# Optimization experiments

Hardware: AMD Instinct MI355X
Metric: run time of the kernel (lower is better)

## Reference

```python
import jax, jax.numpy as jnp
import numpy as np
from math import factorial

# ----- hyperparams (mirror init_kwargs) -----
HIDDEN = [(32,0,1),(32,0,-1),(8,1,1),(8,1,-1),(4,2,1),(4,2,-1)]  # (mul, l, parity)
SCALAR = [(32,0,1)]
SH_IRR = [(1,0,1),(1,1,-1),(1,2,1)]  # spherical harmonics 0e+1o+2e
EMB, NUM_RBF, R_MAX, MLP_DIM, D_IN = 32, 16, 10.0, 256, 64
N_NODES, N_EDGES, N_GRAPHS = 2048, 8192, 8
EDGE_FEATS_DIM = NUM_RBF + 2*EMB

def _slices(irs):
    s, o = [], 0
    for m, l, _ in irs:
        s.append(o); o += m*(2*l+1)
    return s

def _su2_cg(j1, j2, j3, m1, m2, m3):
    if m1 + m2 != m3:
        return 0.0
    f = factorial
    pref = ((2*j3+1)*f(j3+j1-j2)*f(j3-j1+j2)*f(j1+j2-j3)/f(j1+j2+j3+1))**0.5
    pref *= (f(j3+m3)*f(j3-m3)*f(j1-m1)*f(j1+m1)*f(j2-m2)*f(j2+m2))**0.5
    s = 0.0
    for k in range(0, j1+j2-j3+1):
        if j1-m1-k < 0 or j2+m2-k < 0 or j3-j2+m1+k < 0 or j3-j1-m2+k < 0:
            continue
        s += (-1.0)**k/(f(k)*f(j1+j2-j3-k)*f(j1-m1-k)*f(j2+m2-k)*f(j3-j2+m1+k)*f(j3-j1-m2+k))
    return pref*s

def _q(l):  # real -> complex change of basis (e3nn convention incl. (-i)^l phase)
    q = np.zeros((2*l+1, 2*l+1), dtype=np.complex128)
    for m in range(-l, 0):
        q[l+m, l+abs(m)] = 2**-0.5
        q[l+m, l-abs(m)] = -1j*2**-0.5
    q[l, l] = 1.0
    for m in range(1, l+1):
        q[l+m, l+abs(m)] = (-1)**m*2**-0.5
        q[l+m, l-abs(m)] = 1j*(-1)**m*2**-0.5
    return (-1j)**l*q

def _real_cg(l1, l2, l3):  # real-basis Clebsch-Gordan, unit Frobenius norm (wigner-3j-like)
    C = np.zeros((2*l1+1, 2*l2+1, 2*l3+1), dtype=np.complex128)
    for m1 in range(-l1, l1+1):
        for m2 in range(-l2, l2+1):
            m3 = m1 + m2
            if abs(m3) <= l3:
                C[l1+m1, l2+m2, l3+m3] = _su2_cg(l1, l2, l3, m1, m2, m3)
    w = np.einsum('ai,bj,ck,abc->ijk', _q(l1), _q(l2), np.conj(_q(l3)), C)
    re, im = np.real(w), np.imag(w)
    w = re if np.linalg.norm(re) >= np.linalg.norm(im) else im
    return (w/np.linalg.norm(w)).astype(np.float32)

_CG = {}
def cg(l1, l2, l3):
    if (l1, l2, l3) not in _CG:
        _CG[(l1, l2, l3)] = jnp.asarray(_real_cg(l1, l2, l3))
    return _CG[(l1, l2, l3)]

def _build_layer(ir_in, ir_out):  # FullyConnectedTensorProduct path enumeration
    si = _slices(ir_in)
    paths, woff, fan = [], 0, [0]*len(ir_out)
    for i1, (m1, l1, p1) in enumerate(ir_in):
        for (_, l2, p2) in SH_IRR:
            for i3, (m3, l3, p3) in enumerate(ir_out):
                if p1*p2 == p3 and abs(l1-l2) <= l3 <= l1+l2:
                    paths.append((si[i1], m1, l1, l2, i3, m3, l3, woff))
                    fan[i3] += m1
                    woff += m1*m3
    return paths, woff, fan, ir_out

L_SPECS = [_build_layer(SCALAR, HIDDEN), _build_layer(HIDDEN, HIDDEN),
           _build_layer(HIDDEN, HIDDEN), _build_layer(HIDDEN, SCALAR)]
W_NUMELS = [s[1] for s in L_SPECS]  # [1408, 4320, 4320, 1408]

def spherical_harmonics(u):  # component-normalized real SH, l=0,1,2, on unit vectors
    xc, yc, zc = u[:, 0], u[:, 1], u[:, 2]
    s3, s15, s5 = 3**0.5, 15**0.5, 5**0.5
    return jnp.stack([jnp.ones_like(xc),
                      s3*yc, s3*zc, s3*xc,
                      s15*xc*yc, s15*yc*zc, s5*0.5*(3*zc*zc-1.0), s15*xc*zc,
                      s15*0.5*(xc*xc-yc*yc)], axis=1)

def tp_messages(x, sh, w, spec):  # per-edge equivariant tensor product with edge-dep weights
    paths, _, fan, ir_out = spec
    E = x.shape[0]
    outs = [jnp.zeros((E, m*(2*l+1)), x.dtype) for m, l, _ in ir_out]
    for (o1, m1, l1, l2, i3, m3, l3, woff) in paths:
        xp = x[:, o1:o1+m1*(2*l1+1)].reshape(E, m1, 2*l1+1)
        shp = sh[:, l2*l2:(l2+1)*(l2+1)]
        wp = w[:, woff:woff+m1*m3].reshape(E, m1, m3)
        alpha = float(np.sqrt((2*l3+1)/fan[i3]))  # component/element path normalization
        y = alpha*jnp.einsum('eui,ej,euv,ijk->evk', xp, shp, wp, cg(l1, l2, l3))
        outs[i3] = outs[i3] + y.reshape(E, -1)
    return jnp.concatenate(outs, axis=1)

def batch_norm(h, ir_out, eps=1e-5):  # e3nn-style equivariant batch norm (train stats, identity affine)
    outs, o = [], 0
    for m, l, _ in ir_out:
        d = m*(2*l+1)
        f = h[:, o:o+d].reshape(-1, m, 2*l+1); o += d
        if l == 0:
            f = f - f.mean(axis=0, keepdims=True)
        norm2 = (f*f).mean(axis=(0, 2), keepdims=True)
        outs.append((f*jax.lax.rsqrt(norm2+eps)).reshape(h.shape[0], -1))
    return jnp.concatenate(outs, axis=1)

def scatter_mean(msg, idx, n):
    s = jax.ops.segment_sum(msg, idx, num_segments=n)
    c = jax.ops.segment_sum(jnp.ones((idx.shape[0], 1), msg.dtype), idx, num_segments=n)
    return s/jnp.maximum(c, 1.0)

def _forward(x, pos, edge_index, batch, emb_w, emb_b, layer_params):
    ei = jnp.concatenate([edge_index, edge_index[::-1]], axis=1)  # to_undirected (both directions)
    src, dst = ei[0], ei[1]
    h = x@emb_w + emb_b  # (N, 32)
    vec = pos[src] - pos[dst]
    lengths = jnp.linalg.norm(vec, axis=-1)
    sh = spherical_harmonics(vec/lengths[:, None])  # (E, 9)
    mu = jnp.linspace(0.0, R_MAX, NUM_RBF)
    sigma = R_MAX/NUM_RBF
    rbf = jnp.exp(-(((lengths[:, None]-mu)/sigma)**2))  # (E, 16)
    for li, (w1, b1, w2, b2) in enumerate(layer_params):
        ef = jnp.concatenate([rbf, h[src, :EMB], h[dst, :EMB]], axis=1)  # (E, 80)
        w = jax.nn.relu(ef@w1 + b1)@w2 + b2  # per-edge TP weights (dropout=eval noop)
        upd = scatter_mean(tp_messages(h[dst], sh, w, L_SPECS[li]), src, N_NODES)
        upd = batch_norm(upd, L_SPECS[li][3])
        d = upd.shape[-1]
        h_res = h[:, :d] if h.shape[-1] >= d else jnp.pad(h, ((0, 0), (0, d-h.shape[-1])))
        h = upd + h_res  # residual with pad/truncate (F.pad semantics)
    graph = jax.ops.segment_sum(h, batch, num_segments=N_GRAPHS)
    return h, graph

def setup_inputs():
    key = jax.random.key(0)
    ks = jax.random.split(key, 32)
    inp = {}
    inp['x'] = jax.random.normal(ks[0], (N_NODES, D_IN), jnp.float32)
    inp['pos'] = 3.0*jax.random.normal(ks[1], (N_NODES, 3), jnp.float32)
    s = jax.random.randint(ks[2], (N_EDGES,), 0, N_NODES)
    d = (s + jax.random.randint(ks[3], (N_EDGES,), 1, N_NODES)) % N_NODES  # no self-loops
    inp['edge_index'] = jnp.stack([s, d]).astype(jnp.int32)
    inp['batch'] = jnp.sort(jax.random.randint(ks[4], (N_NODES,), 0, N_GRAPHS)).astype(jnp.int32)
    inp['emb_w'] = jax.random.normal(ks[5], (D_IN, EMB), jnp.float32)/np.sqrt(D_IN)
    inp['emb_b'] = jnp.zeros((EMB,), jnp.float32)
    k = 6
    for i, wn in enumerate(W_NUMELS):
        inp[f'l{i}_w1'] = jax.random.normal(ks[k], (EDGE_FEATS_DIM, MLP_DIM), jnp.float32)/np.sqrt(EDGE_FEATS_DIM); k += 1
        inp[f'l{i}_b1'] = jnp.zeros((MLP_DIM,), jnp.float32)
        inp[f'l{i}_w2'] = jax.random.normal(ks[k], (MLP_DIM, wn), jnp.float32)/np.sqrt(MLP_DIM); k += 1
        inp[f'l{i}_b2'] = jnp.zeros((wn,), jnp.float32)
    return inp

def reference(x, pos, edge_index, batch, emb_w, emb_b,
              l0_w1, l0_b1, l0_w2, l0_b2, l1_w1, l1_b1, l1_w2, l1_b2,
              l2_w1, l2_b1, l2_w2, l2_b2, l3_w1, l3_b1, l3_w2, l3_b2):
    lp = [(l0_w1, l0_b1, l0_w2, l0_b2), (l1_w1, l1_b1, l1_w2, l1_b2),
          (l2_w1, l2_b1, l2_w2, l2_b2), (l3_w1, l3_b1, l3_w2, l3_b2)]
    return _forward(x, pos, edge_index, batch, emb_w, emb_b, lp)
```

## Files before the change

kernel.cpp:

```cpp
#include <hip/hip_runtime.h>
#include <hip/hip_bf16.h>
#include <math.h>

#define NNODES 2048
#define NEDG   8192
#define E2     16384
#define NGRAPH 8
#define HSTR   152

static const int LD_DIN[4]  = {32,152,152,152};
static const int LD_DOUT[4] = {152,152,152,32};
static const int LD_WN[4]   = {1408,4320,4320,1408};
static const int LD_WNP[4]  = {1408,4352,4352,1408};
static const int LD_NCH[4]  = {88,88,88,32};
static const int LD_RES[4]  = {32,152,152,152};
#define WNP_MAX 4352

#define SLOT_MAX    1088
#define CELL_N      20
#define SEG_S_N     164
#define SEG_ENT_MAX 1024

typedef short bf16x8 __attribute__((ext_vector_type(8)));
typedef float f32x4  __attribute__((ext_vector_type(4)));

constexpr double cfact(int n){ double r=1.0; for(int i=2;i<=n;i++) r*=(double)i; return r; }
constexpr double csqrt(double x){
  if(x<=0.0) return 0.0;
  double g = x>1.0? x:1.0;
  for(int i=0;i<64;i++) g=0.5*(g+x/g);
  return g;
}
constexpr double csu2cg(int j1,int j2,int j3,int m1,int m2,int m3){
  if(m1+m2!=m3) return 0.0;
  double pref = csqrt((double)(2*j3+1)*cfact(j3+j1-j2)*cfact(j3-j1+j2)*cfact(j1+j2-j3)/cfact(j1+j2+j3+1));
  pref *= csqrt(cfact(j3+m3)*cfact(j3-m3)*cfact(j1-m1)*cfact(j1+m1)*cfact(j2-m2)*cfact(j2+m2));
  double s=0.0;
  for(int k=0;k<=j1+j2-j3;k++){
    if(j1-m1-k<0||j2+m2-k<0||j3-j2+m1+k<0||j3-j1-m2+k<0) continue;
    double t=1.0/(cfact(k)*cfact(j1+j2-j3-k)*cfact(j1-m1-k)*cfact(j2+m2-k)*cfact(j3-j2+m1+k)*cfact(j3-j1-m2+k));
    s += (k&1)? -t : t;
  }
  return pref*s;
}
struct QM { double r[25]; double i[25]; };
constexpr QM cqmat(int l){
  QM q{};
  const double inv2=0.7071067811865476;
  for(int m=-l;m<0;m++){
    int am=-m;
    q.r[(l+m)*5+(l+am)] = inv2;
    q.i[(l+m)*5+(l-am)] = -inv2;
  }
  q.r[l*5+l]=1.0;
  for(int m=1;m<=l;m++){
    double sgn=(m&1)? -1.0:1.0;
    q.r[(l+m)*5+(l+m)] = sgn*inv2;
    q.i[(l+m)*5+(l-m)] = sgn*inv2;
  }
  for(int rep=0;rep<l;rep++){
    for(int t=0;t<25;t++){ double a=q.r[t], b=q.i[t]; q.r[t]=b; q.i[t]=-a; }
  }
  return q;
}
struct CGCell { float v[125]; };
constexpr CGCell mkcell(int l1,int l2,int l3){
  CGCell out{};
  int lo = l1>l2? l1-l2 : l2-l1;
  if(l3<lo || l3>l1+l2) return out;
  QM q1=cqmat(l1), q2=cqmat(l2), q3=cqmat(l3);
  int n1=2*l1+1,n2=2*l2+1,n3=2*l3+1;
  double C[125]={};
  for(int a=0;a<n1;a++)for(int b=0;b<n2;b++)for(int c=0;c<n3;c++)
    C[a*25+b*5+c]=csu2cg(l1,l2,l3,a-l1,b-l2,c-l3);
  double wr[125]={}, wi[125]={};
  for(int i=0;i<n1;i++)for(int j=0;j<n2;j++)for(int k=0;k<n3;k++){
    double ar=0.0, ai=0.0;
    for(int a=0;a<n1;a++)for(int b=0;b<n2;b++){
      double p1r=q1.r[a*5+i], p1i=q1.i[a*5+i];
      double p2r=q2.r[b*5+j], p2i=q2.i[b*5+j];
      double pr=p1r*p2r-p1i*p2i, pi=p1r*p2i+p1i*p2r;
      for(int c=0;c<n3;c++){
        double cv=C[a*25+b*5+c]; if(cv==0.0) continue;
        double p3r=q3.r[c*5+k], p3i=-q3.i[c*5+k];
        ar += (pr*p3r-pi*p3i)*cv;
        ai += (pr*p3i+pi*p3r)*cv;
      }
    }
    wr[i*25+j*5+k]=ar; wi[i*25+j*5+k]=ai;
  }
  double sr=0.0, si=0.0;
  for(int t=0;t<125;t++){ sr+=wr[t]*wr[t]; si+=wi[t]*wi[t]; }
  double nr=csqrt(sr), ni=csqrt(si);
  bool use_re = nr>=ni;
  double nn = use_re? nr:ni;
  double inv = (nn>1e-300)? 1.0/nn : 0.0;
  for(int t=0;t<125;t++) out.v[t]=(float)((use_re? wr[t]:wi[t])*inv);
  return out;
}
constexpr CGCell CGc0 =mkcell(0,0,0), CGc1 =mkcell(0,0,1), CGc2 =mkcell(0,0,2);
constexpr CGCell CGc3 =mkcell(0,1,0), CGc4 =mkcell(0,1,1), CGc5 =mkcell(0,1,2);
constexpr CGCell CGc6 =mkcell(0,2,0), CGc7 =mkcell(0,2,1), CGc8 =mkcell(0,2,2);
constexpr CGCell CGc9 =mkcell(1,0,0), CGc10=mkcell(1,0,1), CGc11=mkcell(1,0,2);
constexpr CGCell CGc12=mkcell(1,1,0), CGc13=mkcell(1,1,1), CGc14=mkcell(1,1,2);
constexpr CGCell CGc15=mkcell(1,2,0), CGc16=mkcell(1,2,1), CGc17=mkcell(1,2,2);
constexpr CGCell CGc18=mkcell(2,0,0), CGc19=mkcell(2,0,1), CGc20=mkcell(2,0,2);
constexpr CGCell CGc21=mkcell(2,1,0), CGc22=mkcell(2,1,1), CGc23=mkcell(2,1,2);
constexpr CGCell CGc24=mkcell(2,2,0), CGc25=mkcell(2,2,1), CGc26=mkcell(2,2,2);
__constant__ CGCell g_cg[27] = {
  CGc0,CGc1,CGc2,CGc3,CGc4,CGc5,CGc6,CGc7,CGc8,
  CGc9,CGc10,CGc11,CGc12,CGc13,CGc14,CGc15,CGc16,CGc17,
  CGc18,CGc19,CGc20,CGc21,CGc22,CGc23,CGc24,CGc25,CGc26};

#define IRH_INIT {{32,0,1},{32,0,-1},{8,1,1},{8,1,-1},{4,2,1},{4,2,-1}}
#define IRS_INIT {{32,0,1}}
#define SH2_INIT {{0,1},{1,-1},{2,1}}

struct PathB { int x_off,m1,d1,sh_off,d2,d3,m3,woff,out_sl,cg_idx,zbase,i3,cell; float alpha; };

__global__ __launch_bounds__(256) void build_tables_kernel(
    unsigned* __restrict__ slot_tab, unsigned* __restrict__ cell_tab,
    int* __restrict__ seg_start, unsigned* __restrict__ seg_ent,
    float* __restrict__ seg_alpha, int* __restrict__ perm){
  __shared__ PathB P[32];
  __shared__ int npath_s, zcount_s, wn_s, ncell_s;
  __shared__ int cellcg[16];
  __shared__ int vals[256];
  __shared__ int part[256];
  int tid=threadIdx.x;
  int li=blockIdx.x;
  if(tid==0){
    const int IRH[6][3]=IRH_INIT;
    const int IRS[1][3]=IRS_INIT;
    const int SH2[3][2]=SH2_INIT;
    const int (*irin)[3]  = (li==0)? IRS: IRH; int nin =(li==0)?1:6;
    const int (*irout)[3] = (li==3)? IRS: IRH; int nout=(li==3)?1:6;
    int si_in[6], si_out[6];
    { int o=0; for(int i=0;i<nin;i++){ si_in[i]=o;  o+=irin[i][0]*(2*irin[i][1]+1);} }
    { int o=0; for(int i=0;i<nout;i++){ si_out[i]=o; o+=irout[i][0]*(2*irout[i][1]+1);} }
    int fan[6]={0,0,0,0,0,0};
    int np=0, woff=0, zb=0, nc=0;
    for(int i1=0;i1<nin;i1++){
      int m1=irin[i1][0], l1=irin[i1][1], p1=irin[i1][2];
      for(int s=0;s<3;s++){
        int l2=SH2[s][0], p2=SH2[s][1];
        for(int i3=0;i3<nout;i3++){
          int m3=irout[i3][0], l3=irout[i3][1], p3=irout[i3][2];
          int lo = l1>l2? l1-l2 : l2-l1;
          if(p1*p2==p3 && l3>=lo && l3<=l1+l2){
            PathB pr;
            pr.x_off=si_in[i1]; pr.m1=m1; pr.d1=2*l1+1;
            pr.sh_off=l2*l2; pr.d2=2*l2+1; pr.d3=2*l3+1;
            pr.m3=m3; pr.woff=woff; pr.out_sl=si_out[i3];
            pr.cg_idx=l1*9+l2*3+l3; pr.zbase=zb; pr.i3=i3; pr.alpha=0.f;
            int ci=-1;
            for(int c=0;c<nc;c++) if(cellcg[c]==pr.cg_idx) ci=c;
            if(ci<0){ cellcg[nc]=pr.cg_idx; ci=nc++; }
            pr.cell=ci;
            P[np++]=pr;
            fan[i3]+=m1; woff+=m1*m3; zb+=m1*(2*l3+1);
          }
        }
      }
    }
    for(int p=0;p<np;p++)
      P[p].alpha=(float)sqrt((double)(2*((P[p].d3-1)/2)+1)/(double)fan[P[p].i3]);
    npath_s=np; zcount_s=zb; wn_s=woff; ncell_s=nc;
  }
  __syncthreads();
  int np=npath_s, zc=zcount_s, nc=ncell_s, wn=wn_s;
  for(int c=tid;c<nc;c+=256){
    int cgi=cellcg[c];
    int l2=(cgi/3)%3;
    cell_tab[li*CELL_N+c]=(unsigned)cgi | ((unsigned)(l2*l2)<<8) | ((unsigned)(2*l2+1)<<12);
  }
  for(int s=tid;s<zc;s+=256){
    int p=0; while(p+1<np && P[p+1].zbase<=s) p++;
    int rel=s-P[p].zbase;
    int k=rel/P[p].m1, u=rel-k*P[p].m1;
    slot_tab[li*SLOT_MAX+s]=(unsigned)(P[p].x_off+u*P[p].d1) | ((unsigned)k<<9) | ((unsigned)P[p].cell<<12);
  }
  int* pm=perm+li*WNP_MAX;
  for(int j=tid;j<wn;j+=256){
    int p=0; while(p+1<np && P[p+1].woff<=j) p++;
    int rel=j-P[p].woff;
    int v=rel/P[p].m1, u=rel%P[p].m1;
    pm[j]=P[p].woff+u*P[p].m3+v;
  }
  int Dout=(li==3)?32:152;
  for(int d=tid;d<Dout;d+=256){
    int cnt=0;
    for(int p=0;p<np;p++){
      int rel=d-P[p].out_sl;
      if(rel>=0 && rel<P[p].m3*P[p].d3) cnt++;
    }
    vals[d]=cnt;
  }
  __syncthreads();
  int v0=(tid<Dout)? vals[tid]:0;
  part[tid]=v0;
  __syncthreads();
  for(int ofs=1;ofs<256;ofs<<=1){
    int v=(tid>=ofs)? part[tid-ofs]:0;
    __syncthreads();
    part[tid]+=v;
    __syncthreads();
  }
  int* sst=seg_start+li*SEG_S_N;
  if(tid<Dout) sst[tid]=part[tid]-v0;
  if(tid==0) sst[Dout]=part[255];
  __syncthreads();
  unsigned* se=seg_ent+li*SEG_ENT_MAX;
  float* sa=seg_alpha+li*SEG_ENT_MAX;
  for(int d=tid;d<Dout;d+=256){
    int pos=sst[d];
    for(int p=0;p<np;p++){
      int rel=d-P[p].out_sl;
      if(rel>=0 && rel<P[p].m3*P[p].d3){
        int v=rel/P[p].d3, k=rel%P[p].d3;
        unsigned z0=(unsigned)(P[p].zbase+k*P[p].m1);
        unsigned w0=(unsigned)(P[p].woff+v*P[p].m1);
        unsigned code=(P[p].m1==32)?2u:((P[p].m1==8)?1u:0u);
        se[pos]= z0 | (w0<<11) | (code<<24);
        sa[pos]=P[p].alpha;
        pos++;
      }
    }
  }
}

static void host_enum(int li, int& zc, int& nseg, int& nc){
  const int IRH[6][3]=IRH_INIT;
  const int IRS[1][3]=IRS_INIT;
  const int SH2[3][2]=SH2_INIT;
  const int (*irin)[3]  = (li==0)? IRS: IRH; int nin =(li==0)?1:6;
  const int (*irout)[3] = (li==3)? IRS: IRH; int nout=(li==3)?1:6;
  zc=0; nseg=0; nc=0;
  int cells[32];
  for(int i1=0;i1<nin;i1++){
    int m1=irin[i1][0], l1=irin[i1][1], p1=irin[i1][2];
    for(int s=0;s<3;s++){
      int l2=SH2[s][0], p2=SH2[s][1];
      for(int i3=0;i3<nout;i3++){
        int m3=irout[i3][0], l3=irout[i3][1], p3=irout[i3][2];
        int lo = l1>l2? l1-l2 : l2-l1;
        if(p1*p2==p3 && l3>=lo && l3<=l1+l2){
          zc+=m1*(2*l3+1); nseg+=m3*(2*l3+1);
          int cg=l1*9+l2*3+l3; int ci=-1;
          for(int c=0;c<nc;c++) if(cells[c]==cg) ci=c;
          if(ci<0) cells[nc++]=cg;
        }
      }
    }
  }
}

__global__ void geom_kernel(const float* __restrict__ pos, const int* __restrict__ ei,
                            int* __restrict__ src2, int* __restrict__ dst2,
                            float* __restrict__ sh, float* __restrict__ rbf,
                            int* __restrict__ counts){
  int e=blockIdx.x*256+threadIdx.x;
  if(e>=E2) return;
  int s,d;
  if(e<NEDG){ s=ei[e]; d=ei[NEDG+e]; }
  else { int j=e-NEDG; s=ei[NEDG+j]; d=ei[j]; }
  src2[e]=s; dst2[e]=d;
  atomicAdd(&counts[s],1);
  float vx=pos[s*3+0]-pos[d*3+0];
  float vy=pos[s*3+1]-pos[d*3+1];
  float vz=pos[s*3+2]-pos[d*3+2];
  float len=sqrtf(vx*vx+vy*vy+vz*vz);
  float inv=1.f/len;
  float x=vx*inv, y=vy*inv, z=vz*inv;
  const float s3=1.7320508075688772f, s15=3.872983346207417f, s5=2.23606797749979f;
  float* shp=sh+(size_t)e*9;
  shp[0]=1.f; shp[1]=s3*y; shp[2]=s3*z; shp[3]=s3*x;
  shp[4]=s15*x*y; shp[5]=s15*y*z; shp[6]=s5*0.5f*(3.f*z*z-1.f);
  shp[7]=s15*x*z; shp[8]=s15*0.5f*(x*x-y*y);
  float* rp=rbf+(size_t)e*16;
  const float invsig=1.6f;
  for(int k=0;k<16;k++){
    float t=(len-(10.0f/15.0f)*(float)k)*invsig;
    rp[k]=expf(-t*t);
  }
}

__global__ void scan_kernel(const int* __restrict__ counts, int* __restrict__ row_ptr){
  __shared__ int part[256];
  int t=threadIdx.x;
  int base=t*8;
  int loc[8]; int s=0;
  #pragma unroll
  for(int i=0;i<8;i++){ loc[i]=counts[base+i]; s+=loc[i]; }
  part[t]=s; __syncthreads();
  for(int ofs=1; ofs<256; ofs<<=1){
    int v=(t>=ofs)? part[t-ofs]:0;
    __syncthreads();
    part[t]+=v;
    __syncthreads();
  }
  int run=part[t]-s;
  #pragma unroll
  for(int i=0;i<8;i++){ row_ptr[base+i]=run; run+=loc[i]; }
  if(t==255) row_ptr[NNODES]=run;
}

__global__ void csr_fill_kernel(const int* __restrict__ src2, const int* __restrict__ row_ptr,
                                int* __restrict__ cursor, int* __restrict__ eidx){
  int e=blockIdx.x*256+threadIdx.x;
  if(e>=E2) return;
  int s=src2[e];
  int p=atomicAdd(&cursor[s],1);
  eidx[row_ptr[s]+p]=e;
}

__global__ void embed_kernel(const float* __restrict__ x, const float* __restrict__ W,
                             const float* __restrict__ b, float* __restrict__ h){
  int idx=blockIdx.x*256+threadIdx.x;
  int n=idx>>5, j=idx&31;
  float acc=b[j];
  for(int k=0;k<64;k++) acc += x[n*64+k]*W[k*32+j];
  h[(size_t)n*HSTR+j]=acc;
}

__global__ void cast_w2t_kernel(const float* __restrict__ w2, const int* __restrict__ perm,
                                __hip_bfloat16* __restrict__ w2t, int wn, int wn_pad){
  int idx=blockIdx.x*256+threadIdx.x;
  if(idx>=wn_pad*256) return;
  int j=idx>>8, k=idx&255;
  float v=(j<wn)? w2[(size_t)k*wn+perm[j]] : 0.f;
  w2t[idx]=__float2bfloat16(v);
}

__global__ __launch_bounds__(256) void mlp1_kernel(
    const float* __restrict__ h, const float* __restrict__ rbf,
    const int* __restrict__ src2, const int* __restrict__ dst2,
    const float* __restrict__ w1, const float* __restrict__ b1,
    __hip_bfloat16* __restrict__ hidden, int e_start){
  __shared__ float ef[16][80];
  int tid=threadIdx.x;
  int e0=e_start+blockIdx.x*16;
  for(int t=tid;t<16*80;t+=256){
    int el=t/80, k=t-el*80; int ge=e0+el;
    float v;
    if(k<16)      v=rbf[(size_t)ge*16+k];
    else if(k<48) v=h[(size_t)src2[ge]*HSTR+(k-16)];
    else          v=h[(size_t)dst2[ge]*HSTR+(k-48)];
    ef[el][k]=v;
  }
  __syncthreads();
  float acc[16];
  float bv=b1[tid];
  #pragma unroll
  for(int e=0;e<16;e++) acc[e]=bv;
  for(int k=0;k<80;k++){
    float wv=w1[k*256+tid];
    #pragma unroll
    for(int e=0;e<16;e++) acc[e]+=ef[e][k]*wv;
  }
  int le0=blockIdx.x*16;
  #pragma unroll
  for(int e=0;e<16;e++)
    hidden[(size_t)(le0+e)*256+tid]=__float2bfloat16(fmaxf(acc[e],0.f));
}

__global__ __launch_bounds__(256) void mlp2_mfma_kernel(
    const __hip_bfloat16* __restrict__ hidden,
    const __hip_bfloat16* __restrict__ w2t,
    const float* __restrict__ b2, const int* __restrict__ perm,
    __hip_bfloat16* __restrict__ wbuf, int wn, int wn_pad){
  __shared__ __hip_bfloat16 As[128*32];
  __shared__ __hip_bfloat16 Bs[128*32];
  int tid=threadIdx.x;
  int lane=tid&63;
  int m0=blockIdx.x*128, n0=blockIdx.y*128;
  int mw=((tid>>6)&1)*64, nw=(tid>>7)*64;
  f32x4 acc[4][4];
  #pragma unroll
  for(int i=0;i<4;i++)
    #pragma unroll
    for(int j=0;j<4;j++) acc[i][j]=(f32x4){0.f,0.f,0.f,0.f};

  int i0=tid*8, i1=tid*8+2048;
  int ar0=i0>>5, ac0=i0&31, ar1=i1>>5, ac1=i1&31;
  const int q4=lane>>4, c16=lane&15;

  for(int k0=0;k0<256;k0+=32){
    __syncthreads();
    *(uint4*)&As[ar0*32+ac0] = *(const uint4*)&hidden[(size_t)(m0+ar0)*256 + k0 + ac0];
    *(uint4*)&As[ar1*32+ac1] = *(const uint4*)&hidden[(size_t)(m0+ar1)*256 + k0 + ac1];
    *(uint4*)&Bs[ar0*32+ac0] = *(const uint4*)&w2t[(size_t)(n0+ar0)*256 + k0 + ac0];
    *(uint4*)&Bs[ar1*32+ac1] = *(const uint4*)&w2t[(size_t)(n0+ar1)*256 + k0 + ac1];
    __syncthreads();
    bf16x8 af[4], bfr[4];
    #pragma unroll
    for(int mi=0;mi<4;mi++) af[mi]=*(bf16x8*)&As[(mw+mi*16+c16)*32 + q4*8];
    #pragma unroll
    for(int ni=0;ni<4;ni++) bfr[ni]=*(bf16x8*)&Bs[(nw+ni*16+c16)*32 + q4*8];
    #pragma unroll
    for(int mi=0;mi<4;mi++)
      #pragma unroll
      for(int ni=0;ni<4;ni++)
        acc[mi][ni]=__builtin_amdgcn_mfma_f32_16x16x32_bf16(af[mi],bfr[ni],acc[mi][ni],0,0,0);
  }
  #pragma unroll
  for(int ni=0;ni<4;ni++){
    int col=n0+nw+ni*16+c16;
    float bias=(col<wn)? b2[perm[col]]:0.f;
    #pragma unroll
    for(int mi=0;mi<4;mi++){
      int row=m0+mw+mi*16+q4*4;
      #pragma unroll
      for(int rr=0;rr<4;rr++)
        wbuf[(size_t)(row+rr)*wn_pad+col]=__float2bfloat16(acc[mi][ni][rr]+bias);
    }
  }
}

__device__ inline void wave_sync(){
  __builtin_amdgcn_s_waitcnt(0);
  __builtin_amdgcn_wave_barrier();
}

__device__ inline float dot8f(const float* zp, const __hip_bfloat16* wp){
  f32x4 za=*(const f32x4*)zp;
  f32x4 zb=*(const f32x4*)(zp+4);
  uint4 wv=*(const uint4*)wp;
  const __hip_bfloat16* wl=(const __hip_bfloat16*)&wv;
  float s=0.f;
  #pragma unroll
  for(int t=0;t<4;t++) s+=za[t]*__bfloat162float(wl[t]);
  #pragma unroll
  for(int t=0;t<4;t++) s+=zb[t]*__bfloat162float(wl[4+t]);
  return s;
}
__device__ inline float dot4f(const float* zp, const __hip_bfloat16* wp){
  f32x4 za=*(const f32x4*)zp;
  uint2 wv=*(const uint2*)wp;
  const __hip_bfloat16* wl=(const __hip_bfloat16*)&wv;
  float s=0.f;
  #pragma unroll
  for(int t=0;t<4;t++) s+=za[t]*__bfloat162float(wl[t]);
  return s;
}

__global__ __launch_bounds__(256) void tp3_kernel(
    const float* __restrict__ h, const float* __restrict__ sh,
    const __hip_bfloat16* __restrict__ wbuf, const int* __restrict__ dst2,
    const unsigned* __restrict__ slot_tab, const unsigned* __restrict__ cell_tab,
    const int* __restrict__ seg_start, const unsigned* __restrict__ seg_ent,
    const float* __restrict__ seg_alpha,
    float* __restrict__ msg, int e_start, int Din, int Dout, int wstride,
    int zc, int nseg, int nc){
  __shared__ float xrow[4][160];
  __shared__ float shs[4][12];
  __shared__ float zsm[4][1088];
  __shared__ float Tw[4][640];
  __shared__ unsigned slot_l[SLOT_MAX];
  __shared__ unsigned seg_l[736];
  __shared__ float    sega_l[736];
  __shared__ int      sst_l[160];
  int tid=threadIdx.x, w=tid>>6, lane=tid&63;
  for(int t=tid;t<zc;t+=256) slot_l[t]=slot_tab[t];
  for(int t=tid;t<nseg;t+=256){ seg_l[t]=seg_ent[t]; sega_l[t]=seg_alpha[t]; }
  for(int t=tid;t<=Dout;t+=256) sst_l[t]=seg_start[t];
  int le=blockIdx.x*4+w, ge=e_start+le;
  int dn=dst2[ge];
  for(int i=lane;i<Din;i+=64) xrow[w][i]=h[(size_t)dn*HSTR+i];
  for(int i=Din+lane;i<160;i+=64) xrow[w][i]=0.f;
  if(lane<9) shs[w][lane]=sh[(size_t)ge*9+lane];
  __syncthreads();
  float* T=&Tw[w][0];
  for(int t=lane;t<nc*25;t+=64){
    int c=t/25, r=t-c*25, k=r/5, i=r-k*5;
    unsigned cm=cell_tab[c];
    int cgi=cm&255, sho=(cm>>8)&15, d2=(cm>>12)&7;
    const float* cgp=g_cg[cgi].v + i*25 + k;
    float s=0.f;
    for(int j=0;j<d2;j++) s+=cgp[j*5]*shs[w][sho+j];
    T[c*40+k*8+i]=s;
  }
  wave_sync();
  const float* xr=&xrow[w][0];
  for(int s=lane;s<zc;s+=64){
    unsigned st=slot_l[s];
    int xb=st&511, k=(st>>9)&7, c=st>>12;
    const float* Tp=&T[c*40+k*8];
    zsm[w][s]=xr[xb]*Tp[0]+xr[xb+1]*Tp[1]+xr[xb+2]*Tp[2]+xr[xb+3]*Tp[3]+xr[xb+4]*Tp[4];
  }
  wave_sync();
  const __hip_bfloat16* wrow=wbuf+(size_t)le*wstride;
  const float* zbase=&zsm[w][0];
  for(int d=lane;d<Dout;d+=64){
    int s0=sst_l[d], s1=sst_l[d+1];
    float acc=0.f;
    for(int s=s0;s<s1;s++){
      unsigned sg=seg_l[s];
      float al=sega_l[s];
      int z0=sg&2047, w0=(sg>>11)&8191, code=sg>>24;
      const float* zp=zbase+z0;
      const __hip_bfloat16* wp=wrow+w0;
      float ds;
      if(code==2){
        ds=0.f;
        #pragma unroll
        for(int t=0;t<4;t++) ds+=dot8f(zp+t*8,wp+t*8);
      } else if(code==1){
        ds=dot8f(zp,wp);
      } else {
        ds=dot4f(zp,wp);
      }
      acc+=al*ds;
    }
    msg[(size_t)ge*Dout+d]=acc;
  }
}

__global__ void aggregate_kernel(const float* __restrict__ msg, const int* __restrict__ row_ptr,
                                 const int* __restrict__ eidx, const int* __restrict__ counts,
                                 float* __restrict__ upd, int Dout){
  int n=blockIdx.x; int lane=threadIdx.x;
  int p0=row_ptr[n], p1=row_ptr[n+1];
  int c=counts[n]; if(c<1) c=1;
  float inv=1.f/(float)c;
  for(int d=lane;d<Dout;d+=64){
    float s=0.f;
    for(int p=p0;p<p1;p++) s+=msg[(size_t)eidx[p]*Dout+d];
    upd[(size_t)n*Dout+d]=s*inv;
  }
}

__device__ inline int hidden_chan_of_dim(int d){
  if(d<64)  return d;
  if(d<88)  return 64+(d-64)/3;
  if(d<112) return 72+(d-88)/3;
  if(d<132) return 80+(d-112)/5;
  return 84+(d-132)/5;
}
__device__ inline void hidden_chan_params(int c, int& off, int& dk, int& l0){
  if(c<64){ off=c; dk=1; l0=1; }
  else if(c<72){ off=64+(c-64)*3; dk=3; l0=0; }
  else if(c<80){ off=88+(c-72)*3; dk=3; l0=0; }
  else if(c<84){ off=112+(c-80)*5; dk=5; l0=0; }
  else { off=132+(c-84)*5; dk=5; l0=0; }
}

__global__ void stats_kernel(const float* __restrict__ upd, float* __restrict__ stats,
                             int Dout, int scalar_out){
  int c=blockIdx.x, tid=threadIdx.x;
  int off,dk,l0;
  if(scalar_out){ off=c; dk=1; l0=1; }
  else hidden_chan_params(c,off,dk,l0);
  float s=0.f, s2=0.f;
  int total=NNODES*dk;
  for(int t=tid;t<total;t+=256){
    int n=t/dk, k=t-n*dk;
    float v=upd[(size_t)n*Dout+off+k];
    s+=v; s2+=v*v;
  }
  __shared__ float rs[256], rs2[256];
  rs[tid]=s; rs2[tid]=s2; __syncthreads();
  for(int o=128;o>0;o>>=1){
    if(tid<o){ rs[tid]+=rs[tid+o]; rs2[tid]+=rs2[tid+o]; }
    __syncthreads();
  }
  if(tid==0){
    float cnt=(float)total;
    float mean = l0? rs[0]/cnt : 0.f;
    float var = rs2[0]/cnt - mean*mean;
    stats[c*2]=mean;
    stats[c*2+1]=1.0f/sqrtf(var+1e-5f);
  }
}

__global__ void apply_kernel(const float* __restrict__ upd, const float* __restrict__ stats,
                             const float* __restrict__ h_cur, float* __restrict__ h_next,
                             int Dout, int res_dim, int scalar_out, int out_stride){
  int idx=blockIdx.x*256+threadIdx.x;
  if(idx>=NNODES*Dout) return;
  int n=idx/Dout, d=idx-n*Dout;
  int c = scalar_out? d : hidden_chan_of_dim(d);
  float v=(upd[idx]-stats[2*c])*stats[2*c+1];
  float res=(d<res_dim)? h_cur[(size_t)n*HSTR+d] : 0.f;
  h_next[(size_t)n*out_stride+d]=v+res;
}

__global__ void graph_kernel(const float* __restrict__ hfin, const int* __restrict__ batch,
                             float* __restrict__ gout){
  int idx=blockIdx.x*256+threadIdx.x;
  int n=idx>>5, d=idx&31;
  atomicAdd(&gout[batch[n]*32+d], hfin[idx]);
}

extern "C" void kernel_launch(void* const* d_in, const int* in_sizes, int n_in,
                              void* d_out, int out_size, void* d_ws, size_t ws_size,
                              hipStream_t stream){
  (void)in_sizes; (void)n_in; (void)out_size;
  const float* x    =(const float*)d_in[0];
  const float* pos  =(const float*)d_in[1];
  const int*   ei   =(const int*)d_in[2];
  const int*   batch=(const int*)d_in[3];
  const float* emb_w=(const float*)d_in[4];
  const float* emb_b=(const float*)d_in[5];
  const float *W1[4], *B1[4], *W2[4], *B2[4];
  for(int l=0;l<4;l++){
    W1[l]=(const float*)d_in[6+4*l];
    B1[l]=(const float*)d_in[7+4*l];
    W2[l]=(const float*)d_in[8+4*l];
    B2[l]=(const float*)d_in[9+4*l];
  }
  int ZC[4], NSEG[4], NC[4];
  for(int l=0;l<4;l++) host_enum(l,ZC[l],NSEG[l],NC[l]);

  char* base=(char*)d_ws;
  size_t off=0;
  auto alloc=[&](size_t bytes)->char*{
    off=(off+255)&~(size_t)255;
    char* p=base+off; off+=bytes; return p;
  };
  float*  h_a   =(float*)alloc((size_t)NNODES*HSTR*4);
  float*  h_b   =(float*)alloc((size_t)NNODES*HSTR*4);
  float*  shb   =(float*)alloc((size_t)E2*9*4);
  float*  rbfb  =(float*)alloc((size_t)E2*16*4);
  int*    src2  =(int*)  alloc((size_t)E2*4);
  int*    dst2  =(int*)  alloc((size_t)E2*4);
  int*    counts=(int*)  alloc((size_t)NNODES*4);
  int*    cursor=(int*)  alloc((size_t)NNODES*4);
  int*    row_ptr=(int*) alloc((size_t)(NNODES+4)*4);
  int*    eidx  =(int*)  alloc((size_t)E2*4);
  float*  msg   =(float*)alloc((size_t)E2*HSTR*4);
  float*  upd   =(float*)alloc((size_t)NNODES*HSTR*4);
  float*  stats =(float*)alloc(256*4);
  unsigned* slot_tab=(unsigned*)alloc((size_t)4*SLOT_MAX*4);
  unsigned* cell_tg =(unsigned*)alloc((size_t)4*CELL_N*4);
  int*      seg_s   =(int*)     alloc((size_t)4*SEG_S_N*4);
  unsigned* seg_e   =(unsigned*)alloc((size_t)4*SEG_ENT_MAX*4);
  float*    seg_a   =(float*)   alloc((size_t)4*SEG_ENT_MAX*4);
  int*      perm    =(int*)     alloc((size_t)4*WNP_MAX*4);
  __hip_bfloat16* w2t[4];
  for(int l=0;l<4;l++) w2t[l]=(__hip_bfloat16*)alloc((size_t)LD_WNP[l]*256*2);

  int E_CHUNK=E2;
  while(E_CHUNK>128){
    size_t need=off;
    need=(need+255)&~(size_t)255; need+=(size_t)E_CHUNK*256*2;
    need=(need+255)&~(size_t)255; need+=(size_t)E_CHUNK*WNP_MAX*2;
    if(need<=ws_size) break;
    E_CHUNK>>=1;
  }
  __hip_bfloat16* hidden=(__hip_bfloat16*)alloc((size_t)E_CHUNK*256*2);
  __hip_bfloat16* wbuf  =(__hip_bfloat16*)alloc((size_t)E_CHUNK*WNP_MAX*2);

  hipMemsetAsync(counts,0,(size_t)NNODES*4,stream);
  hipMemsetAsync(cursor,0,(size_t)NNODES*4,stream);
  build_tables_kernel<<<4,256,0,stream>>>(slot_tab,cell_tg,seg_s,seg_e,seg_a,perm);
  geom_kernel<<<E2/256,256,0,stream>>>(pos,ei,src2,dst2,shb,rbfb,counts);
  scan_kernel<<<1,256,0,stream>>>(counts,row_ptr);
  csr_fill_kernel<<<E2/256,256,0,stream>>>(src2,row_ptr,cursor,eidx);
  embed_kernel<<<(NNODES*32)/256,256,0,stream>>>(x,emb_w,emb_b,h_a);
  for(int l=0;l<4;l++)
    cast_w2t_kernel<<<(LD_WNP[l]*256+255)/256,256,0,stream>>>(W2[l],perm+l*WNP_MAX,w2t[l],LD_WN[l],LD_WNP[l]);

  float* h_cur=h_a; float* h_nxt=h_b;
  for(int li=0;li<4;li++){
    int wn=LD_WN[li], wnp=LD_WNP[li], Din=LD_DIN[li], Dout=LD_DOUT[li];
    for(int e0=0;e0<E2;e0+=E_CHUNK){
      mlp1_kernel<<<E_CHUNK/16,256,0,stream>>>(h_cur,rbfb,src2,dst2,W1[li],B1[li],hidden,e0);
      dim3 g2(E_CHUNK/128, wnp/128);
      mlp2_mfma_kernel<<<g2,256,0,stream>>>(hidden,w2t[li],B2[li],perm+li*WNP_MAX,wbuf,wn,wnp);
      tp3_kernel<<<E_CHUNK/4,256,0,stream>>>(h_cur,shb,wbuf,dst2,
          slot_tab+li*SLOT_MAX, cell_tg+li*CELL_N,
          seg_s+li*SEG_S_N, seg_e+li*SEG_ENT_MAX, seg_a+li*SEG_ENT_MAX,
          msg,e0,Din,Dout,wnp, ZC[li], NSEG[li], NC[li]);
    }
    aggregate_kernel<<<NNODES,64,0,stream>>>(msg,row_ptr,eidx,counts,upd,Dout);
    stats_kernel<<<LD_NCH[li],256,0,stream>>>(upd,stats,Dout,li==3?1:0);
    int tot=NNODES*Dout;
    if(li<3)
      apply_kernel<<<(tot+255)/256,256,0,stream>>>(upd,stats,h_cur,h_nxt,Dout,LD_RES[li],0,HSTR);
    else
      apply_kernel<<<(tot+255)/256,256,0,stream>>>(upd,stats,h_cur,(float*)d_out,Dout,LD_RES[li],1,32);
    float* tmp=h_cur; h_cur=h_nxt; h_nxt=tmp;
  }

  float* gout=(float*)d_out + (size_t)NNODES*32;
  hipMemsetAsync(gout,0,(size_t)NGRAPH*32*4,stream);
  graph_kernel<<<(NNODES*32)/256,256,0,stream>>>((const float*)d_out,batch,gout);
}
```

Before: 886.0 us.

## Fold path alpha into W2 weights and shrink tensor-product kernel shared memory

Per-path normalization alpha is folded into the permuted, bf16-cast W2 weights and the bias. This removes the per-segment alpha multiply and the seg_alpha table. The tensor-product kernel no longer stages slot and segment tables in shared memory and reads them straight from global memory. Tw is packed densely, so the block-wide barrier becomes a wave sync. Together these cut LDS use to allow higher occupancy, but table reads now hit cache, and folding alpha before the bf16 rounding slightly changes precision.

```diff
diff --git a/kernel.cpp b/kernel.cpp
--- a/kernel.cpp
+++ b/kernel.cpp
@@ -121,7 +121,7 @@
 __global__ __launch_bounds__(256) void build_tables_kernel(
     unsigned* __restrict__ slot_tab, unsigned* __restrict__ cell_tab,
     int* __restrict__ seg_start, unsigned* __restrict__ seg_ent,
-    float* __restrict__ seg_alpha, int* __restrict__ perm){
+    int* __restrict__ perm, float* __restrict__ alpha_col){
   __shared__ PathB P[32];
   __shared__ int npath_s, zcount_s, wn_s, ncell_s;
   __shared__ int cellcg[16];
@@ -181,11 +181,13 @@
     slot_tab[li*SLOT_MAX+s]=(unsigned)(P[p].x_off+u*P[p].d1) | ((unsigned)k<<9) | ((unsigned)P[p].cell<<12);
   }
   int* pm=perm+li*WNP_MAX;
+  float* ac=alpha_col+li*WNP_MAX;
   for(int j=tid;j<wn;j+=256){
     int p=0; while(p+1<np && P[p+1].woff<=j) p++;
     int rel=j-P[p].woff;
     int v=rel/P[p].m1, u=rel%P[p].m1;
     pm[j]=P[p].woff+u*P[p].m3+v;
+    ac[j]=P[p].alpha;
   }
   int Dout=(li==3)?32:152;
   for(int d=tid;d<Dout;d+=256){
@@ -211,7 +213,6 @@
   if(tid==0) sst[Dout]=part[255];
   __syncthreads();
   unsigned* se=seg_ent+li*SEG_ENT_MAX;
-  float* sa=seg_alpha+li*SEG_ENT_MAX;
   for(int d=tid;d<Dout;d+=256){
     int pos=sst[d];
     for(int p=0;p<np;p++){
@@ -222,20 +223,19 @@
         unsigned w0=(unsigned)(P[p].woff+v*P[p].m1);
         unsigned code=(P[p].m1==32)?2u:((P[p].m1==8)?1u:0u);
         se[pos]= z0 | (w0<<11) | (code<<24);
-        sa[pos]=P[p].alpha;
         pos++;
       }
     }
   }
 }
 
-static void host_enum(int li, int& zc, int& nseg, int& nc){
+static void host_enum(int li, int& zc, int& nc){
   const int IRH[6][3]=IRH_INIT;
   const int IRS[1][3]=IRS_INIT;
   const int SH2[3][2]=SH2_INIT;
   const int (*irin)[3]  = (li==0)? IRS: IRH; int nin =(li==0)?1:6;
   const int (*irout)[3] = (li==3)? IRS: IRH; int nout=(li==3)?1:6;
-  zc=0; nseg=0; nc=0;
+  zc=0; nc=0;
   int cells[32];
   for(int i1=0;i1<nin;i1++){
     int m1=irin[i1][0], l1=irin[i1][1], p1=irin[i1][2];
@@ -245,7 +245,7 @@
         int m3=irout[i3][0], l3=irout[i3][1], p3=irout[i3][2];
         int lo = l1>l2? l1-l2 : l2-l1;
         if(p1*p2==p3 && l3>=lo && l3<=l1+l2){
-          zc+=m1*(2*l3+1); nseg+=m3*(2*l3+1);
+          zc+=m1*(2*l3+1);
           int cg=l1*9+l2*3+l3; int ci=-1;
           for(int c=0;c<nc;c++) if(cells[c]==cg) ci=c;
           if(ci<0) cells[nc++]=cg;
@@ -324,11 +324,12 @@
 }
 
 __global__ void cast_w2t_kernel(const float* __restrict__ w2, const int* __restrict__ perm,
+                                const float* __restrict__ alpha_col,
                                 __hip_bfloat16* __restrict__ w2t, int wn, int wn_pad){
   int idx=blockIdx.x*256+threadIdx.x;
   if(idx>=wn_pad*256) return;
   int j=idx>>8, k=idx&255;
-  float v=(j<wn)? w2[(size_t)k*wn+perm[j]] : 0.f;
+  float v=(j<wn)? w2[(size_t)k*wn+perm[j]]*alpha_col[j] : 0.f;
   w2t[idx]=__float2bfloat16(v);
 }
 
@@ -368,6 +369,7 @@
     const __hip_bfloat16* __restrict__ hidden,
     const __hip_bfloat16* __restrict__ w2t,
     const float* __restrict__ b2, const int* __restrict__ perm,
+    const float* __restrict__ alpha_col,
     __hip_bfloat16* __restrict__ wbuf, int wn, int wn_pad){
   __shared__ __hip_bfloat16 As[128*32];
   __shared__ __hip_bfloat16 Bs[128*32];
@@ -406,7 +408,7 @@
   #pragma unroll
   for(int ni=0;ni<4;ni++){
     int col=n0+nw+ni*16+c16;
-    float bias=(col<wn)? b2[perm[col]]:0.f;
+    float bias=(col<wn)? b2[perm[col]]*alpha_col[col]:0.f;
     #pragma unroll
     for(int mi=0;mi<4;mi++){
       int row=m0+mw+mi*16+q4*4;
@@ -444,32 +446,24 @@
   return s;
 }
 
-__global__ __launch_bounds__(256) void tp3_kernel(
+__global__ __launch_bounds__(256) void tp4_kernel(
     const float* __restrict__ h, const float* __restrict__ sh,
     const __hip_bfloat16* __restrict__ wbuf, const int* __restrict__ dst2,
     const unsigned* __restrict__ slot_tab, const unsigned* __restrict__ cell_tab,
     const int* __restrict__ seg_start, const unsigned* __restrict__ seg_ent,
-    const float* __restrict__ seg_alpha,
     float* __restrict__ msg, int e_start, int Din, int Dout, int wstride,
-    int zc, int nseg, int nc){
+    int zc, int nc){
   __shared__ float xrow[4][160];
   __shared__ float shs[4][12];
   __shared__ float zsm[4][1088];
-  __shared__ float Tw[4][640];
-  __shared__ unsigned slot_l[SLOT_MAX];
-  __shared__ unsigned seg_l[736];
-  __shared__ float    sega_l[736];
-  __shared__ int      sst_l[160];
+  __shared__ float Tw[4][376];
   int tid=threadIdx.x, w=tid>>6, lane=tid&63;
-  for(int t=tid;t<zc;t+=256) slot_l[t]=slot_tab[t];
-  for(int t=tid;t<nseg;t+=256){ seg_l[t]=seg_ent[t]; sega_l[t]=seg_alpha[t]; }
-  for(int t=tid;t<=Dout;t+=256) sst_l[t]=seg_start[t];
   int le=blockIdx.x*4+w, ge=e_start+le;
   int dn=dst2[ge];
   for(int i=lane;i<Din;i+=64) xrow[w][i]=h[(size_t)dn*HSTR+i];
   for(int i=Din+lane;i<160;i+=64) xrow[w][i]=0.f;
   if(lane<9) shs[w][lane]=sh[(size_t)ge*9+lane];
-  __syncthreads();
+  wave_sync();
   float* T=&Tw[w][0];
   for(int t=lane;t<nc*25;t+=64){
     int c=t/25, r=t-c*25, k=r/5, i=r-k*5;
@@ -478,39 +472,35 @@
     const float* cgp=g_cg[cgi].v + i*25 + k;
     float s=0.f;
     for(int j=0;j<d2;j++) s+=cgp[j*5]*shs[w][sho+j];
-    T[c*40+k*8+i]=s;
+    T[t]=s;
   }
   wave_sync();
   const float* xr=&xrow[w][0];
   for(int s=lane;s<zc;s+=64){
-    unsigned st=slot_l[s];
+    unsigned st=slot_tab[s];
     int xb=st&511, k=(st>>9)&7, c=st>>12;
-    const float* Tp=&T[c*40+k*8];
+    const float* Tp=&T[c*25+k*5];
     zsm[w][s]=xr[xb]*Tp[0]+xr[xb+1]*Tp[1]+xr[xb+2]*Tp[2]+xr[xb+3]*Tp[3]+xr[xb+4]*Tp[4];
   }
   wave_sync();
   const __hip_bfloat16* wrow=wbuf+(size_t)le*wstride;
   const float* zbase=&zsm[w][0];
   for(int d=lane;d<Dout;d+=64){
-    int s0=sst_l[d], s1=sst_l[d+1];
+    int s0=seg_start[d], s1=seg_start[d+1];
     float acc=0.f;
     for(int s=s0;s<s1;s++){
-      unsigned sg=seg_l[s];
-      float al=sega_l[s];
+      unsigned sg=seg_ent[s];
       int z0=sg&2047, w0=(sg>>11)&8191, code=sg>>24;
       const float* zp=zbase+z0;
       const __hip_bfloat16* wp=wrow+w0;
-      float ds;
       if(code==2){
-        ds=0.f;
         #pragma unroll
-        for(int t=0;t<4;t++) ds+=dot8f(zp+t*8,wp+t*8);
+        for(int t=0;t<4;t++) acc+=dot8f(zp+t*8,wp+t*8);
       } else if(code==1){
-        ds=dot8f(zp,wp);
+        acc+=dot8f(zp,wp);
       } else {
-        ds=dot4f(zp,wp);
+        acc+=dot4f(zp,wp);
       }
-      acc+=al*ds;
     }
     msg[(size_t)ge*Dout+d]=acc;
   }
@@ -609,8 +599,8 @@
     W2[l]=(const float*)d_in[8+4*l];
     B2[l]=(const float*)d_in[9+4*l];
   }
-  int ZC[4], NSEG[4], NC[4];
-  for(int l=0;l<4;l++) host_enum(l,ZC[l],NSEG[l],NC[l]);
+  int ZC[4], NC[4];
+  for(int l=0;l<4;l++) host_enum(l,ZC[l],NC[l]);
 
   char* base=(char*)d_ws;
   size_t off=0;
@@ -635,8 +625,8 @@
   unsigned* cell_tg =(unsigned*)alloc((size_t)4*CELL_N*4);
   int*      seg_s   =(int*)     alloc((size_t)4*SEG_S_N*4);
   unsigned* seg_e   =(unsigned*)alloc((size_t)4*SEG_ENT_MAX*4);
-  float*    seg_a   =(float*)   alloc((size_t)4*SEG_ENT_MAX*4);
   int*      perm    =(int*)     alloc((size_t)4*WNP_MAX*4);
+  float*    alpha_c =(float*)   alloc((size_t)4*WNP_MAX*4);
   __hip_bfloat16* w2t[4];
   for(int l=0;l<4;l++) w2t[l]=(__hip_bfloat16*)alloc((size_t)LD_WNP[l]*256*2);
 
@@ -653,13 +643,14 @@
 
   hipMemsetAsync(counts,0,(size_t)NNODES*4,stream);
   hipMemsetAsync(cursor,0,(size_t)NNODES*4,stream);
-  build_tables_kernel<<<4,256,0,stream>>>(slot_tab,cell_tg,seg_s,seg_e,seg_a,perm);
+  build_tables_kernel<<<4,256,0,stream>>>(slot_tab,cell_tg,seg_s,seg_e,perm,alpha_c);
   geom_kernel<<<E2/256,256,0,stream>>>(pos,ei,src2,dst2,shb,rbfb,counts);
   scan_kernel<<<1,256,0,stream>>>(counts,row_ptr);
   csr_fill_kernel<<<E2/256,256,0,stream>>>(src2,row_ptr,cursor,eidx);
   embed_kernel<<<(NNODES*32)/256,256,0,stream>>>(x,emb_w,emb_b,h_a);
   for(int l=0;l<4;l++)
-    cast_w2t_kernel<<<(LD_WNP[l]*256+255)/256,256,0,stream>>>(W2[l],perm+l*WNP_MAX,w2t[l],LD_WN[l],LD_WNP[l]);
+    cast_w2t_kernel<<<(LD_WNP[l]*256+255)/256,256,0,stream>>>(
+        W2[l],perm+l*WNP_MAX,alpha_c+l*WNP_MAX,w2t[l],LD_WN[l],LD_WNP[l]);
 
   float* h_cur=h_a; float* h_nxt=h_b;
   for(int li=0;li<4;li++){
@@ -667,11 +658,12 @@
     for(int e0=0;e0<E2;e0+=E_CHUNK){
       mlp1_kernel<<<E_CHUNK/16,256,0,stream>>>(h_cur,rbfb,src2,dst2,W1[li],B1[li],hidden,e0);
       dim3 g2(E_CHUNK/128, wnp/128);
-      mlp2_mfma_kernel<<<g2,256,0,stream>>>(hidden,w2t[li],B2[li],perm+li*WNP_MAX,wbuf,wn,wnp);
-      tp3_kernel<<<E_CHUNK/4,256,0,stream>>>(h_cur,shb,wbuf,dst2,
+      mlp2_mfma_kernel<<<g2,256,0,stream>>>(hidden,w2t[li],B2[li],perm+li*WNP_MAX,
+                                            alpha_c+li*WNP_MAX,wbuf,wn,wnp);
+      tp4_kernel<<<E_CHUNK/4,256,0,stream>>>(h_cur,shb,wbuf,dst2,
           slot_tab+li*SLOT_MAX, cell_tg+li*CELL_N,
-          seg_s+li*SEG_S_N, seg_e+li*SEG_ENT_MAX, seg_a+li*SEG_ENT_MAX,
-          msg,e0,Din,Dout,wnp, ZC[li], NSEG[li], NC[li]);
+          seg_s+li*SEG_S_N, seg_e+li*SEG_ENT_MAX,
+          msg,e0,Din,Dout,wnp, ZC[li], NC[li]);
     }
     aggregate_kernel<<<NNODES,64,0,stream>>>(msg,row_ptr,eidx,counts,upd,Dout);
     stats_kernel<<<LD_NCH[li],256,0,stream>>>(upd,stats,Dout,li==3?1:0);
```

Result: faster. 836.5 us (-5.6%).
